# Kernel optimization log

Measured on AMD Instinct MI355X. Metric: run time of the kernel, lower is better.

## Reference

```python
import jax, jax.numpy as jnp
import numpy as np

V = 6          # num_variables
K = 6          # codebook_size
D = 32         # embedding_dim
C = 3          # channels
B = 64         # batch
N = K ** V     # 46656 codebook combinations
EPS = 1e-5     # torch BatchNorm eps
ENTROPY_SCALE = 0.1


def setup_inputs() -> dict:
    key = jax.random.key(0)
    ks = jax.random.split(key, 40)
    i = iter(range(40))
    def rn(shape, s):
        return jax.random.normal(ks[next(i)], shape, dtype=jnp.float32) * s
    def rv(shape):
        return 0.5 + 0.5 * jax.random.uniform(ks[next(i)], shape, dtype=jnp.float32)
    inp = {
        'x': jax.random.normal(ks[next(i)], (B, C, 7, 7), dtype=jnp.float32),
        # encoder
        'conv_w': rn((256, C, 7, 7), 0.08), 'conv_b': rn((256,), 0.01),
        'ebn2_g': 1.0 + rn((256,), 0.1), 'ebn2_b': rn((256,), 0.1),
        'fc1_w': rn((1024, 256), 0.06), 'fc1_b': rn((1024,), 0.01),
        'ebn1_g': 1.0 + rn((1024,), 0.1), 'ebn1_b': rn((1024,), 0.1),
        'fc2_w': rn((V * K, 1024), 0.03), 'fc2_b': rn((V * K,), 0.01),
        # quantizer embeddings (V separate codebooks)
        'embeds': jax.random.normal(ks[next(i)], (V, K, D), dtype=jnp.float32),
        # decoder
        'dfc1_w': rn((1024, V * D), 0.07), 'dfc1_b': rn((1024,), 0.01),
        'dbn1_g': 1.0 + rn((1024,), 0.1), 'dbn1_b': rn((1024,), 0.1),
        'dbn1_rm': rn((1024,), 0.1), 'dbn1_rv': rv((1024,)),
        'dfc2_w': rn((256, 1024), 0.03), 'dfc2_b': rn((256,), 0.01),
        'dbn2_g': 1.0 + rn((256,), 0.1), 'dbn2_b': rn((256,), 0.1),
        'dbn2_rm': rn((256,), 0.1), 'dbn2_rv': rv((256,)),
        'dct1_w': rn((256, 16, 7, 7), 0.05), 'dct1_b': rn((16,), 0.01),
        'dbn3_g': 1.0 + rn((16,), 0.1), 'dbn3_b': rn((16,), 0.1),
        'dbn3_rm': rn((16,), 0.1), 'dbn3_rv': rv((16,)),
        'dct2_w': rn((16, C), 0.2), 'dct2_b': rn((C,), 0.01),
    }
    return inp


def _bn_eval(t, g, b, rm, rvar):
    # eval-mode BatchNorm (running stats); params broadcast over leading dims
    return g * (t - rm) * jax.lax.rsqrt(rvar + EPS) + b


def _bn_train(t, g, b):
    # train-mode BatchNorm1d on (B, F): biased batch statistics over dim 0
    m = t.mean(0)
    v = ((t - m) ** 2).mean(0)
    return g * (t - m) * jax.lax.rsqrt(v + EPS) + b


def _decode_all(embeds, dfc1_w, dfc1_b, dbn1_g, dbn1_b, dbn1_rm, dbn1_rv,
                dfc2_w, dfc2_b, dbn2_g, dbn2_b, dbn2_rm, dbn2_rv,
                dct1_w, dct1_b, dbn3_g, dbn3_b, dbn3_rm, dbn3_rv,
                dct2_w, dct2_b):
    # enumerate all K^V index tuples in itertools.product order (first var slowest)
    idx = jnp.arange(N)
    powers = K ** (V - 1 - jnp.arange(V))
    combos = (idx[:, None] // powers[None, :]) % K          # (N, V)
    z = embeds[jnp.arange(V)[None, :], combos]              # (N, V, D) gather
    h = z.reshape(N, V * D) @ dfc1_w.T + dfc1_b             # (N, 1024)
    h = jax.nn.relu(_bn_eval(h, dbn1_g, dbn1_b, dbn1_rm, dbn1_rv))
    h = h @ dfc2_w.T + dfc2_b                               # (N, 256)
    h = jax.nn.relu(_bn_eval(h, dbn2_g, dbn2_b, dbn2_rm, dbn2_rv))
    # ConvTranspose2d(256,16,7,stride=2) on 1x1 input == einsum with full kernel
    h = jnp.einsum('ni,iohw->nohw', h, dct1_w) + dct1_b[:, None, None]  # (N,16,7,7)
    h = jax.nn.relu(_bn_eval(h, dbn3_g[:, None, None], dbn3_b[:, None, None],
                             dbn3_rm[:, None, None], dbn3_rv[:, None, None]))
    # ConvTranspose2d(16,C,1,1) == pointwise channel mix
    em = jnp.einsum('nihw,io->nohw', h, dct2_w) + dct2_b[:, None, None]  # (N,C,7,7)
    return em


def reference(x, conv_w, conv_b, ebn2_g, ebn2_b, fc1_w, fc1_b, ebn1_g, ebn1_b,
              fc2_w, fc2_b, embeds, dfc1_w, dfc1_b, dbn1_g, dbn1_b, dbn1_rm,
              dbn1_rv, dfc2_w, dfc2_b, dbn2_g, dbn2_b, dbn2_rm, dbn2_rv,
              dct1_w, dct1_b, dbn3_g, dbn3_b, dbn3_rm, dbn3_rv, dct2_w, dct2_b):
    # emission means for every codebook combination (batched decode, BN eval)
    em = _decode_all(embeds, dfc1_w, dfc1_b, dbn1_g, dbn1_b, dbn1_rm, dbn1_rv,
                     dfc2_w, dfc2_b, dbn2_g, dbn2_b, dbn2_rm, dbn2_rv,
                     dct1_w, dct1_b, dbn3_g, dbn3_b, dbn3_rm, dbn3_rv,
                     dct2_w, dct2_b)                         # (N, C, 7, 7)
    # encoder: Conv2d(C,256,7) on 7x7 input collapses to a single GEMM
    e = jnp.einsum('bchw,ochw->bo', x, conv_w) + conv_b      # (B, 256)
    e = jax.nn.relu(_bn_train(e, ebn2_g, ebn2_b))
    e = e @ fc1_w.T + fc1_b                                  # (B, 1024)
    e = jax.nn.relu(_bn_train(e, ebn1_g, ebn1_b))
    logits = e @ fc2_w.T + fc2_b                             # (B, V*K)
    # quantizer
    latent_dist = jax.nn.softmax(logits.reshape(B, V, K), axis=-1)
    latent_loss = ENTROPY_SCALE * jnp.sum(
        latent_dist * jnp.log(latent_dist + 1e-10), axis=(1, 2))
    # obs logits: -0.5 * ||em - x||^2 summed over (C,H,W), via expanded form
    E = em.reshape(N, -1)                                    # (N, 147)
    X = x.reshape(B, -1)                                     # (B, 147)
    obs = -0.5 * (jnp.sum(E * E, -1)[None, :]
                  - 2.0 * (X @ E.T)
                  + jnp.sum(X * X, -1)[:, None])             # (B, N)
    obs_logits = obs.reshape((B,) + (K,) * V)
    return obs_logits, latent_dist, latent_loss
```

## Files before the change

### kernel.cpp

```cpp
#include <hip/hip_runtime.h>
#include <math.h>

#define EPSF 1e-5f
#define NNC 46656

typedef __attribute__((ext_vector_type(4))) float  f32x4;
typedef __attribute__((ext_vector_type(8))) short  short8;
typedef __attribute__((ext_vector_type(8))) unsigned short ushort8;
typedef __attribute__((ext_vector_type(4))) unsigned int uint4v;

__device__ __forceinline__ float bf2f(unsigned short u) {
    unsigned int x = ((unsigned int)u) << 16;
    return __builtin_bit_cast(float, x);
}
__device__ __forceinline__ unsigned short f2bf(float f) {
    unsigned int x = __builtin_bit_cast(unsigned int, f);
    unsigned int r = (x + 0x7fffu + ((x >> 16) & 1u)) >> 16;
    return (unsigned short)r;
}

__device__ __forceinline__ short8 packrelu8(ushort8 H8, ushort8 S8) {
    uint4v H = __builtin_bit_cast(uint4v, H8);
    uint4v S = __builtin_bit_cast(uint4v, S8);
    uint4v O;
#pragma unroll
    for (int d = 0; d < 4; ++d) {
        float hlo = __builtin_bit_cast(float, H[d] << 16);
        float hhi = __builtin_bit_cast(float, H[d] & 0xffff0000u);
        float slo = __builtin_bit_cast(float, S[d] << 16);
        float shi = __builtin_bit_cast(float, S[d] & 0xffff0000u);
        unsigned int rlo = __builtin_bit_cast(unsigned int, fmaxf(hlo + slo, 0.f));
        unsigned int rhi = __builtin_bit_cast(unsigned int, fmaxf(hhi + shi, 0.f));
        O[d] = __builtin_amdgcn_perm(rhi, rlo, 0x07060302u);
    }
    return __builtin_bit_cast(short8, O);
}

#define WS_SH    37888u
#define WS_S3    148480u
#define WS_W2BF  259072u
#define WS_C2    390144u
#define WS_W3BF  390400u
#define WS_C3    490752u
#define WS_XBF   490768u
#define WS_SX2   495888u
#define WS_E1T   495952u
#define WS_E2T   512336u
#define WS_FLAG  577872u

#define OBS_SIZE (64*NNC)
#define DIST_OFF OBS_SIZE
#define LOSS_OFF (OBS_SIZE + 64*36)

#define LDS_BYTES 75008


__global__ void dvae_k1(const float* __restrict__ x,
                        const float* __restrict__ conv_w, const float* __restrict__ conv_b,
                        const float* __restrict__ ebn2_g, const float* __restrict__ ebn2_b,
                        const float* __restrict__ embeds, const float* __restrict__ dfc1_w,
                        const float* __restrict__ dfc1_b,
                        const float* __restrict__ dbn1_g, const float* __restrict__ dbn1_b,
                        const float* __restrict__ dbn1_rm, const float* __restrict__ dbn1_rv,
                        const float* __restrict__ dfc2_w, const float* __restrict__ dfc2_b,
                        const float* __restrict__ dbn2_g, const float* __restrict__ dbn2_b,
                        const float* __restrict__ dbn2_rm, const float* __restrict__ dbn2_rv,
                        const float* __restrict__ dct1_w, const float* __restrict__ dct1_b,
                        const float* __restrict__ dbn3_g, const float* __restrict__ dbn3_b,
                        const float* __restrict__ dbn3_rm, const float* __restrict__ dbn3_rv,
                        float* __restrict__ ws) {
    __shared__ float sbuf[12544];
    int bx = blockIdx.x, tid = threadIdx.x;
    if (bx < 64) {
        float* wtile = sbuf;
        float* semb  = sbuf + 3088;
        float* Pt    = sbuf + 4240;
        float* c1s   = sbuf + 4960;
        int j0 = bx * 16;
        for (int e = tid; e < 16 * 192; e += 256)
            wtile[(e / 192) * 193 + (e % 192)] = dfc1_w[j0 * 192 + e];
        for (int e = tid; e < 1152; e += 256) semb[e] = embeds[e];
        __syncthreads();
        for (int e = tid; e < 576; e += 256) {
            int vk = e >> 4, jL = e & 15;
            int v = vk / 6;
            int j = j0 + jL;
            const float* wrow = &wtile[jL * 193 + v * 32];
            const float* ep = &semb[vk * 32];
            float dot = 0.f;
#pragma unroll
            for (int d = 0; d < 32; ++d) dot += wrow[d] * ep[d];
            float s1 = dbn1_g[j] * rsqrtf(dbn1_rv[j] + EPSF);
            Pt[vk * 20 + jL] = s1 * dot;
        }
        if (tid < 16) {
            int j = j0 + tid;
            float s = dbn1_g[j] * rsqrtf(dbn1_rv[j] + EPSF);
            c1s[tid] = s * dfc1_b[j] + dbn1_b[j] - dbn1_rm[j] * s;
        }
        __syncthreads();
        unsigned short* Sh = (unsigned short*)(ws + WS_SH);
        unsigned short* S3 = (unsigned short*)(ws + WS_S3);
        for (int e = tid; e < 216 * 16; e += 256) {
            int gh = e >> 4, jL = e & 15;
            int d0 = gh / 36, d1 = (gh / 6) % 6, d2 = gh % 6;
            float vh = c1s[jL] + Pt[d0 * 20 + jL] + Pt[(6 + d1) * 20 + jL] + Pt[(12 + d2) * 20 + jL];
            float vs = Pt[(18 + d0) * 20 + jL] + Pt[(24 + d1) * 20 + jL] + Pt[(30 + d2) * 20 + jL];
            Sh[gh * 1024 + j0 + jL] = f2bf(vh);
            S3[gh * 1024 + j0 + jL] = f2bf(vs);
        }
    } else if (bx < 320) {
        int t = (bx - 64) * 256 + tid;
        int i = t >> 8, kq = (t & 255) * 4;
        float s2 = dbn2_g[i] * rsqrtf(dbn2_rv[i] + EPSF);
        float4 w = *(const float4*)(dfc2_w + i * 1024 + kq);
        unsigned short* dst = (unsigned short*)(ws + WS_W2BF) + i * 1024 + kq;
        dst[0] = f2bf(s2 * w.x); dst[1] = f2bf(s2 * w.y);
        dst[2] = f2bf(s2 * w.z); dst[3] = f2bf(s2 * w.w);
        if (kq == 0) ws[WS_C2 + i] = s2 * dfc2_b[i] + dbn2_b[i] - dbn2_rm[i] * s2;
    } else if (bx < 336) {
        int blk = bx - 320;
        for (int e = tid; e < 12544; e += 256) sbuf[e] = dct1_w[blk * 12544 + e];
        __syncthreads();
        unsigned short* W3 = (unsigned short*)(ws + WS_W3BF);
        for (int e = tid; e < 1568; e += 256) {
            int up = e >> 1, k8 = (e & 1) * 8;
            int o = up & 15, hw = up >> 4;
            float s3 = dbn3_g[o] * rsqrtf(dbn3_rv[o] + EPSF);
            ushort8 ov;
#pragma unroll
            for (int t2 = 0; t2 < 8; ++t2)
                ov[t2] = f2bf(s3 * sbuf[(k8 + t2) * 784 + o * 49 + hw]);
            *(ushort8*)(W3 + up * 256 + blk * 16 + k8) = ov;
        }
        if (blk == 0 && tid < 16) {
            float s = dbn3_g[tid] * rsqrtf(dbn3_rv[tid] + EPSF);
            ws[WS_C3 + tid] = s * dct1_b[tid] + dbn3_b[tid] - dbn3_rm[tid] * s;
        }
    } else if (bx == 336) {
        unsigned short* Xb = (unsigned short*)(ws + WS_XBF);
        if (tid == 0) *(int*)(ws + WS_FLAG) = 0;
        if (tid < 64) {
            const float* xp = x + tid * 147;
            float s = 0.f;
            for (int qq = 0; qq < 147; ++qq) { float v = xp[qq]; s += v * v; }
            ws[WS_SX2 + tid] = s;
        }
        for (int e = tid; e < 64 * 160; e += 256) {
            int b = e / 160, col = e % 160;
            float v = 0.f;
            if (col < 147) { int hw = col / 3, c = col % 3; v = x[b * 147 + c * 49 + hw]; }
            Xb[e] = f2bf(v);
        }
    } else {
        int blk = bx - 337;
        for (int e = tid; e < 9408; e += 256) sbuf[e] = x[e];
        __syncthreads();
        int b = tid & 63;
        int oL = __builtin_amdgcn_readfirstlane(tid >> 6);
        int o = blk * 4 + oL;
        const float* wp = conv_w + o * 147;
        float acc = conv_b[o];
#pragma unroll 7
        for (int qq = 0; qq < 147; ++qq) acc += sbuf[b * 147 + qq] * wp[qq];
        float m = acc;
#pragma unroll
        for (int s = 1; s < 64; s <<= 1) m += __shfl_xor(m, s);
        m *= (1.f / 64.f);
        float d = acc - m;
        float var = d * d;
#pragma unroll
        for (int s = 1; s < 64; s <<= 1) var += __shfl_xor(var, s);
        var *= (1.f / 64.f);
        float y = ebn2_g[o] * d * rsqrtf(var + EPSF) + ebn2_b[o];
        ws[WS_E1T + o * 64 + b] = fmaxf(y, 0.f);
    }
}


__launch_bounds__(256, 2)
__global__ void dvae_k3(const unsigned short* __restrict__ Sh,
                        const unsigned short* __restrict__ S3g,
                        const unsigned short* __restrict__ W2,
                        const float* __restrict__ c2g,
                        const unsigned short* __restrict__ W3,
                        const float* __restrict__ c3g,
                        const float* __restrict__ d2wg,
                        const float* __restrict__ d2bg,
                        const unsigned short* __restrict__ Xg,
                        const float* __restrict__ sx2g,
                        const float* __restrict__ fc1_w, const float* __restrict__ fc1_b,
                        const float* __restrict__ ebn1_g, const float* __restrict__ ebn1_b,
                        const float* __restrict__ e1T,
                        float* __restrict__ e2T,
                        int* __restrict__ flag,
                        const float* __restrict__ fc2_w,
                        const float* __restrict__ fc2_b,
                        float* __restrict__ out) {
    extern __shared__ char sm[];
    int tid = threadIdx.x;

    if (blockIdx.x < 256) {
        int blk = blockIdx.x;
        int b = tid & 63;
        int jL = __builtin_amdgcn_readfirstlane(tid >> 6);
        int j = blk * 4 + jL;
        const float* wp = fc1_w + j * 256;
        float acc = fc1_b[j];
#pragma unroll 8
        for (int o = 0; o < 256; ++o) acc += e1T[o * 64 + b] * wp[o];
        float m = acc;
#pragma unroll
        for (int s = 1; s < 64; s <<= 1) m += __shfl_xor(m, s);
        m *= (1.f / 64.f);
        float d = acc - m;
        float var = d * d;
#pragma unroll
        for (int s = 1; s < 64; s <<= 1) var += __shfl_xor(var, s);
        var *= (1.f / 64.f);
        float y = ebn1_g[j] * d * rsqrtf(var + EPSF) + ebn1_b[j];
        e2T[j * 64 + b] = fmaxf(y, 0.f);
        __syncthreads();
        if (tid == 0) { __threadfence(); atomicAdd(flag, 1); }
        return;
    }

    if (blockIdx.x == 256) {
        if (tid == 0) {
            while (atomicAdd(flag, 0) < 256) __builtin_amdgcn_s_sleep(8);
        }
        __syncthreads();
        float* wch = (float*)sm;
        float* ech = (float*)(sm + 18432);
        float* LG  = (float*)(sm + 51200);
        int b = tid & 63;
        int wvU = __builtin_amdgcn_readfirstlane(tid >> 6);
        float accv[9];
#pragma unroll
        for (int it = 0; it < 9; ++it) accv[it] = 0.f;
        for (int ch = 0; ch < 8; ++ch) {
            __syncthreads();
            for (int e = tid; e < 36 * 128; e += 256)
                wch[e] = fc2_w[(e >> 7) * 1024 + ch * 128 + (e & 127)];
            for (int e = tid; e < 128 * 64; e += 256)
                ech[e] = e2T[(ch * 128 + (e >> 6)) * 64 + (e & 63)];
            __syncthreads();
            for (int jl = 0; jl < 128; ++jl) {
                float ev = ech[jl * 64 + b];
#pragma unroll
                for (int it = 0; it < 9; ++it)
                    accv[it] += ev * wch[(wvU + it * 4) * 128 + jl];
            }
        }
#pragma unroll
        for (int it = 0; it < 9; ++it) {
            int o = wvU + it * 4;
            LG[b * 36 + o] = accv[it] + fc2_b[o];
        }
        __syncthreads();
        if (tid < 64) {
            float loss = 0.f;
#pragma unroll
            for (int v = 0; v < 6; ++v) {
                float mx = -1e30f;
#pragma unroll
                for (int k = 0; k < 6; ++k) mx = fmaxf(mx, LG[tid * 36 + v * 6 + k]);
                float s = 0.f, ex[6];
#pragma unroll
                for (int k = 0; k < 6; ++k) { ex[k] = expf(LG[tid * 36 + v * 6 + k] - mx); s += ex[k]; }
                float inv = 1.f / s;
#pragma unroll
                for (int k = 0; k < 6; ++k) {
                    float dd = ex[k] * inv;
                    out[DIST_OFF + tid * 36 + v * 6 + k] = dd;
                    loss += dd * logf(dd + 1e-10f);
                }
            }
            out[LOSS_OFF + tid] = 0.1f * loss;
        }
        return;
    }

    int wv = tid >> 6, lane = tid & 63, l15 = lane & 15, q = lane >> 4;
    int db = blockIdx.x - 257;
    int g0 = (db / 27) * 8, r0 = (db % 27) * 8;
    float* sE2p = (float*)(sm + 0);
    float* sE2f = (float*)(sm + 1024);
    unsigned short* emL = (unsigned short*)(sm + 1280);
    float* h3w = (float*)(sm + 21760 + wv * 5120);
    unsigned short* h2L = (unsigned short*)(sm + 42240);
    char* Ast = sm + 1280;

    f32x4 acc[4][4];
#pragma unroll
    for (int a = 0; a < 4; ++a)
#pragma unroll
        for (int b = 0; b < 4; ++b) acc[a][b] = (f32x4){0.f, 0.f, 0.f, 0.f};

    int gh_t = g0 + (lane >> 3);
    int r_t  = r0 + (lane & 7);
    const unsigned short* shp = Sh  + gh_t * 1024 + wv * 32;
    const unsigned short* s3p = S3g + r_t  * 1024 + wv * 32;
    const unsigned short* bbase = W2 + (wv * 64 + l15) * 1024 + q * 8;
    int Xw = (lane & 7) << 4;
    int Xr = (l15 & 7) << 4;

    ushort8 rsh[4], rs3[4];
#pragma unroll
    for (int i = 0; i < 4; ++i) {
        rsh[i] = *(const ushort8*)(shp + i * 8);
        rs3[i] = *(const ushort8*)(s3p + i * 8);
    }
    short8 bpre[4];
#pragma unroll
    for (int j = 0; j < 4; ++j) bpre[j] = *(const short8*)(bbase + j * 16384);
#pragma unroll
    for (int i = 0; i < 4; ++i)
        *(short8*)(Ast + lane * 256 + ((wv * 64 + i * 16) ^ Xw)) = packrelu8(rsh[i], rs3[i]);
    __syncthreads();

    for (int c = 0; c < 8; ++c) {
        int cb = (c & 1) << 14;
        if (c < 7) {
            const unsigned short* p1 = shp + (c + 1) * 128;
            const unsigned short* p3 = s3p + (c + 1) * 128;
#pragma unroll
            for (int i = 0; i < 4; ++i) {
                rsh[i] = *(const ushort8*)(p1 + i * 8);
                rs3[i] = *(const ushort8*)(p3 + i * 8);
            }
        }
#pragma unroll
        for (int ss = 0; ss < 4; ++ss) {
            int s = c * 4 + ss;
            short8 af[4];
#pragma unroll
            for (int mt = 0; mt < 4; ++mt)
                af[mt] = *(const short8*)(Ast + cb + (mt * 16 + l15) * 256 + ((ss * 64 + q * 16) ^ Xr));
            short8 bcur[4];
#pragma unroll
            for (int j = 0; j < 4; ++j) bcur[j] = bpre[j];
            if (s < 31) {
#pragma unroll
                for (int j = 0; j < 4; ++j) bpre[j] = *(const short8*)(bbase + j * 16384 + (s + 1) * 32);
            }
#pragma unroll
            for (int mt = 0; mt < 4; ++mt)
#pragma unroll
                for (int j = 0; j < 4; ++j)
                    acc[mt][j] = __builtin_amdgcn_mfma_f32_16x16x32_bf16(af[mt], bcur[j], acc[mt][j], 0, 0, 0);
        }
        if (c < 7) {
            int nb = ((c + 1) & 1) << 14;
#pragma unroll
            for (int i = 0; i < 4; ++i)
                *(short8*)(Ast + nb + lane * 256 + ((wv * 64 + i * 16) ^ Xw)) = packrelu8(rsh[i], rs3[i]);
        }
        __syncthreads();
    }

#pragma unroll
    for (int j = 0; j < 4; ++j) {
        int i = wv * 64 + j * 16 + l15;
        float cc = c2g[i];
#pragma unroll
        for (int mt = 0; mt < 4; ++mt)
#pragma unroll
            for (int r = 0; r < 4; ++r) {
                int m = mt * 16 + q * 4 + r;
                h2L[((i >> 3) * 64 + m) * 8 + (i & 7)] = f2bf(fmaxf(acc[mt][j][r] + cc, 0.f));
            }
    }
    __syncthreads();

    float c3v = c3g[l15];
    float db0 = d2bg[0], db1 = d2bg[1], db2 = d2bg[2];
    float dw0[16], dw1[16], dw2[16];
#pragma unroll
    for (int o = 0; o < 16; ++o) {
        dw0[o] = d2wg[o * 3 + 0]; dw1[o] = d2wg[o * 3 + 1]; dw2[o] = d2wg[o * 3 + 2];
    }
    float sE2a = 0.f;
    for (int c = wv; c < 13; c += 4) {
        int hw0 = c * 4;
        f32x4 a2[4][4];
#pragma unroll
        for (int a = 0; a < 4; ++a)
#pragma unroll
            for (int b = 0; b < 4; ++b) a2[a][b] = (f32x4){0.f, 0.f, 0.f, 0.f};
        const unsigned short* b3[4];
#pragma unroll
        for (int j = 0; j < 4; ++j) {
            int hw = hw0 + j; if (hw > 48) hw = 48;
            b3[j] = W3 + (hw * 16 + l15) * 256 + q * 8;
        }
        short8 bpre2[4];
#pragma unroll
        for (int j = 0; j < 4; ++j) bpre2[j] = *(const short8*)(b3[j]);
#pragma unroll
        for (int s = 0; s < 8; ++s) {
            short8 bcur[4];
#pragma unroll
            for (int j = 0; j < 4; ++j) bcur[j] = bpre2[j];
            if (s < 7) {
#pragma unroll
                for (int j = 0; j < 4; ++j) bpre2[j] = *(const short8*)(b3[j] + (s + 1) * 32);
            }
            short8 af[4];
#pragma unroll
            for (int mt = 0; mt < 4; ++mt)
                af[mt] = *(const short8*)(h2L + ((s * 4 + q) * 64 + mt * 16 + l15) * 8);
#pragma unroll
            for (int mt = 0; mt < 4; ++mt)
#pragma unroll
                for (int j = 0; j < 4; ++j)
                    a2[mt][j] = __builtin_amdgcn_mfma_f32_16x16x32_bf16(af[mt], bcur[j], a2[mt][j], 0, 0, 0);
        }
#pragma unroll
        for (int j = 0; j < 4; ++j) {
            int hw = hw0 + j;
            if (hw <= 48) {
#pragma unroll
                for (int mt = 0; mt < 4; ++mt)
#pragma unroll
                    for (int r = 0; r < 4; ++r)
                        h3w[(mt * 16 + q * 4 + r) * 20 + l15] = fmaxf(a2[mt][j][r] + c3v, 0.f);
                float hvv[16];
#pragma unroll
                for (int g = 0; g < 4; ++g) {
                    f32x4 tv = *(const f32x4*)(h3w + lane * 20 + g * 4);
                    hvv[g * 4 + 0] = tv[0]; hvv[g * 4 + 1] = tv[1];
                    hvv[g * 4 + 2] = tv[2]; hvv[g * 4 + 3] = tv[3];
                }
                float e0 = db0, e1 = db1, e2 = db2;
#pragma unroll
                for (int o = 0; o < 16; ++o) {
                    e0 += hvv[o] * dw0[o]; e1 += hvv[o] * dw1[o]; e2 += hvv[o] * dw2[o];
                }
                unsigned short u0 = f2bf(e0), u1 = f2bf(e1), u2 = f2bf(e2);
                float f0 = bf2f(u0), f1 = bf2f(u1), f2v = bf2f(u2);
                sE2a += f0 * f0 + f1 * f1 + f2v * f2v;
                emL[lane * 160 + hw * 3 + 0] = u0;
                emL[lane * 160 + hw * 3 + 1] = u1;
                emL[lane * 160 + hw * 3 + 2] = u2;
            }
        }
    }
    sE2p[wv * 64 + lane] = sE2a;
    for (int e = tid; e < 64 * 13; e += 256) emL[(e / 13) * 160 + 147 + (e % 13)] = 0;
    __syncthreads();
    if (tid < 64) sE2f[tid] = sE2p[tid] + sE2p[64 + tid] + sE2p[128 + tid] + sE2p[192 + tid];
    __syncthreads();

    f32x4 aO[4];
#pragma unroll
    for (int j = 0; j < 4; ++j) aO[j] = (f32x4){0.f, 0.f, 0.f, 0.f};
    const unsigned short* xrow = Xg + (wv * 16 + l15) * 160 + q * 8;
#pragma unroll
    for (int s = 0; s < 5; ++s) {
        short8 af = *(const short8*)(xrow + s * 32);
#pragma unroll
        for (int j = 0; j < 4; ++j) {
            short8 bfv = *(const short8*)(emL + (j * 16 + l15) * 160 + s * 32 + q * 8);
            aO[j] = __builtin_amdgcn_mfma_f32_16x16x32_bf16(af, bfv, aO[j], 0, 0, 0);
        }
    }
    int b0 = wv * 16 + q * 4;
    float sxv[4];
#pragma unroll
    for (int r = 0; r < 4; ++r) sxv[r] = sx2g[b0 + r];
#pragma unroll
    for (int j = 0; j < 4; ++j) {
        int rloc = j * 16 + l15;
        int n = (g0 + (rloc >> 3)) * 216 + r0 + (rloc & 7);
        float he = 0.5f * sE2f[rloc];
#pragma unroll
        for (int r = 0; r < 4; ++r)
            out[(size_t)(b0 + r) * NNC + n] = aO[j][r] - he - 0.5f * sxv[r];
    }
}


extern "C" void kernel_launch(void* const* d_in, const int* in_sizes, int n_in,
                              void* d_out, int out_size, void* d_ws, size_t ws_size,
                              hipStream_t stream) {
    const float* x       = (const float*)d_in[0];
    const float* conv_w  = (const float*)d_in[1];
    const float* conv_b  = (const float*)d_in[2];
    const float* ebn2_g  = (const float*)d_in[3];
    const float* ebn2_b  = (const float*)d_in[4];
    const float* fc1_w   = (const float*)d_in[5];
    const float* fc1_b   = (const float*)d_in[6];
    const float* ebn1_g  = (const float*)d_in[7];
    const float* ebn1_b  = (const float*)d_in[8];
    const float* fc2_w   = (const float*)d_in[9];
    const float* fc2_b   = (const float*)d_in[10];
    const float* embeds  = (const float*)d_in[11];
    const float* dfc1_w  = (const float*)d_in[12];
    const float* dfc1_b  = (const float*)d_in[13];
    const float* dbn1_g  = (const float*)d_in[14];
    const float* dbn1_b  = (const float*)d_in[15];
    const float* dbn1_rm = (const float*)d_in[16];
    const float* dbn1_rv = (const float*)d_in[17];
    const float* dfc2_w  = (const float*)d_in[18];
    const float* dfc2_b  = (const float*)d_in[19];
    const float* dbn2_g  = (const float*)d_in[20];
    const float* dbn2_b  = (const float*)d_in[21];
    const float* dbn2_rm = (const float*)d_in[22];
    const float* dbn2_rv = (const float*)d_in[23];
    const float* dct1_w  = (const float*)d_in[24];
    const float* dct1_b  = (const float*)d_in[25];
    const float* dbn3_g  = (const float*)d_in[26];
    const float* dbn3_b  = (const float*)d_in[27];
    const float* dbn3_rm = (const float*)d_in[28];
    const float* dbn3_rv = (const float*)d_in[29];
    const float* dct2_w  = (const float*)d_in[30];
    const float* dct2_b  = (const float*)d_in[31];

    float* ws  = (float*)d_ws;
    float* out = (float*)d_out;

    dvae_k1<<<401, 256, 0, stream>>>(x, conv_w, conv_b, ebn2_g, ebn2_b,
                                     embeds, dfc1_w, dfc1_b, dbn1_g, dbn1_b, dbn1_rm, dbn1_rv,
                                     dfc2_w, dfc2_b, dbn2_g, dbn2_b, dbn2_rm, dbn2_rv,
                                     dct1_w, dct1_b, dbn3_g, dbn3_b, dbn3_rm, dbn3_rv, ws);

    hipFuncSetAttribute(reinterpret_cast<const void*>(dvae_k3),
                        hipFuncAttributeMaxDynamicSharedMemorySize, LDS_BYTES);
    dvae_k3<<<986, 256, LDS_BYTES, stream>>>(
        (const unsigned short*)(ws + WS_SH), (const unsigned short*)(ws + WS_S3),
        (const unsigned short*)(ws + WS_W2BF), ws + WS_C2,
        (const unsigned short*)(ws + WS_W3BF), ws + WS_C3,
        dct2_w, dct2_b,
        (const unsigned short*)(ws + WS_XBF), ws + WS_SX2,
        fc1_w, fc1_b, ebn1_g, ebn1_b,
        ws + WS_E1T, ws + WS_E2T, (int*)(ws + WS_FLAG),
        fc2_w, fc2_b, out);
}
```

Before: 260.6 us.

## Fuse final 16-to-3 projection into MFMA registers and shrink LDS for occupancy

The A/B operands of the third decoder MFMA are swapped, so each lane holds four output channels for one codebook row. The final 16-to-3 transposed-conv projection is then done in registers with cross-quarter shuffles, which removes the per-wave h3w LDS staging buffer. LDS regions are re-aliased (emL at offset 0, sE2p over h2L, LG over wch), the LDS footprint drops, and launch bounds rise to three blocks per CU. The aliasing requires extra barriers and leaves only a quarter of lanes active for the bf16 stores, and the higher occupancy target may force register spilling.

```diff
diff --git a/kernel.cpp b/kernel.cpp
--- a/kernel.cpp
+++ b/kernel.cpp
@@ -52,7 +52,7 @@
 #define DIST_OFF OBS_SIZE
 #define LOSS_OFF (OBS_SIZE + 64*36)
 
-#define LDS_BYTES 75008
+#define LDS_BYTES 53248
 
 
 __global__ void dvae_k1(const float* __restrict__ x,
@@ -178,7 +178,7 @@
 }
 
 
-__launch_bounds__(256, 2)
+__launch_bounds__(256, 3)
 __global__ void dvae_k3(const unsigned short* __restrict__ Sh,
                         const unsigned short* __restrict__ S3g,
                         const unsigned short* __restrict__ W2,
@@ -232,7 +232,7 @@
         __syncthreads();
         float* wch = (float*)sm;
         float* ech = (float*)(sm + 18432);
-        float* LG  = (float*)(sm + 51200);
+        float* LG  = (float*)sm;
         int b = tid & 63;
         int wvU = __builtin_amdgcn_readfirstlane(tid >> 6);
         float accv[9];
@@ -252,6 +252,7 @@
                     accv[it] += ev * wch[(wvU + it * 4) * 128 + jl];
             }
         }
+        __syncthreads();
 #pragma unroll
         for (int it = 0; it < 9; ++it) {
             int o = wvU + it * 4;
@@ -284,12 +285,11 @@
     int wv = tid >> 6, lane = tid & 63, l15 = lane & 15, q = lane >> 4;
     int db = blockIdx.x - 257;
     int g0 = (db / 27) * 8, r0 = (db % 27) * 8;
-    float* sE2p = (float*)(sm + 0);
-    float* sE2f = (float*)(sm + 1024);
-    unsigned short* emL = (unsigned short*)(sm + 1280);
-    float* h3w = (float*)(sm + 21760 + wv * 5120);
-    unsigned short* h2L = (unsigned short*)(sm + 42240);
-    char* Ast = sm + 1280;
+    unsigned short* emL = (unsigned short*)sm;
+    unsigned short* h2L = (unsigned short*)(sm + 20480);
+    float* sE2p = (float*)(sm + 20480);
+    float* sE2f = (float*)(sm + 21504);
+    char* Ast = sm;
 
     f32x4 acc[4][4];
 #pragma unroll
@@ -373,14 +373,18 @@
     }
     __syncthreads();
 
-    float c3v = c3g[l15];
+    float c3q[4], dwq0[4], dwq1[4], dwq2[4];
+#pragma unroll
+    for (int r = 0; r < 4; ++r) {
+        int o = q * 4 + r;
+        c3q[r]  = c3g[o];
+        dwq0[r] = d2wg[o * 3 + 0];
+        dwq1[r] = d2wg[o * 3 + 1];
+        dwq2[r] = d2wg[o * 3 + 2];
+    }
     float db0 = d2bg[0], db1 = d2bg[1], db2 = d2bg[2];
-    float dw0[16], dw1[16], dw2[16];
-#pragma unroll
-    for (int o = 0; o < 16; ++o) {
-        dw0[o] = d2wg[o * 3 + 0]; dw1[o] = d2wg[o * 3 + 1]; dw2[o] = d2wg[o * 3 + 2];
-    }
-    float sE2a = 0.f;
+    float sE2acc[4] = {0.f, 0.f, 0.f, 0.f};
+
     for (int c = wv; c < 13; c += 4) {
         int hw0 = c * 4;
         f32x4 a2[4][4];
@@ -414,39 +418,39 @@
             for (int mt = 0; mt < 4; ++mt)
 #pragma unroll
                 for (int j = 0; j < 4; ++j)
-                    a2[mt][j] = __builtin_amdgcn_mfma_f32_16x16x32_bf16(af[mt], bcur[j], a2[mt][j], 0, 0, 0);
+                    a2[mt][j] = __builtin_amdgcn_mfma_f32_16x16x32_bf16(bcur[j], af[mt], a2[mt][j], 0, 0, 0);
         }
 #pragma unroll
         for (int j = 0; j < 4; ++j) {
             int hw = hw0 + j;
             if (hw <= 48) {
 #pragma unroll
-                for (int mt = 0; mt < 4; ++mt)
-#pragma unroll
-                    for (int r = 0; r < 4; ++r)
-                        h3w[(mt * 16 + q * 4 + r) * 20 + l15] = fmaxf(a2[mt][j][r] + c3v, 0.f);
-                float hvv[16];
-#pragma unroll
-                for (int g = 0; g < 4; ++g) {
-                    f32x4 tv = *(const f32x4*)(h3w + lane * 20 + g * 4);
-                    hvv[g * 4 + 0] = tv[0]; hvv[g * 4 + 1] = tv[1];
-                    hvv[g * 4 + 2] = tv[2]; hvv[g * 4 + 3] = tv[3];
+                for (int mt = 0; mt < 4; ++mt) {
+                    float p0 = 0.f, p1 = 0.f, p2 = 0.f;
+#pragma unroll
+                    for (int r = 0; r < 4; ++r) {
+                        float h = fmaxf(a2[mt][j][r] + c3q[r], 0.f);
+                        p0 += h * dwq0[r]; p1 += h * dwq1[r]; p2 += h * dwq2[r];
+                    }
+                    p0 += __shfl_xor(p0, 16); p0 += __shfl_xor(p0, 32);
+                    p1 += __shfl_xor(p1, 16); p1 += __shfl_xor(p1, 32);
+                    p2 += __shfl_xor(p2, 16); p2 += __shfl_xor(p2, 32);
+                    unsigned short u0 = f2bf(p0 + db0), u1 = f2bf(p1 + db1), u2 = f2bf(p2 + db2);
+                    float f0 = bf2f(u0), f1 = bf2f(u1), f2v = bf2f(u2);
+                    if (q == 0) {
+                        sE2acc[mt] += f0 * f0 + f1 * f1 + f2v * f2v;
+                        unsigned short* er = emL + (mt * 16 + l15) * 160 + hw * 3;
+                        er[0] = u0; er[1] = u1; er[2] = u2;
+                    }
                 }
-                float e0 = db0, e1 = db1, e2 = db2;
-#pragma unroll
-                for (int o = 0; o < 16; ++o) {
-                    e0 += hvv[o] * dw0[o]; e1 += hvv[o] * dw1[o]; e2 += hvv[o] * dw2[o];
-                }
-                unsigned short u0 = f2bf(e0), u1 = f2bf(e1), u2 = f2bf(e2);
-                float f0 = bf2f(u0), f1 = bf2f(u1), f2v = bf2f(u2);
-                sE2a += f0 * f0 + f1 * f1 + f2v * f2v;
-                emL[lane * 160 + hw * 3 + 0] = u0;
-                emL[lane * 160 + hw * 3 + 1] = u1;
-                emL[lane * 160 + hw * 3 + 2] = u2;
-            }
-        }
-    }
-    sE2p[wv * 64 + lane] = sE2a;
+            }
+        }
+    }
+    __syncthreads();
+    if (q == 0) {
+#pragma unroll
+        for (int mt = 0; mt < 4; ++mt) sE2p[wv * 64 + mt * 16 + l15] = sE2acc[mt];
+    }
     for (int e = tid; e < 64 * 13; e += 256) emL[(e / 13) * 160 + 147 + (e % 13)] = 0;
     __syncthreads();
     if (tid < 64) sE2f[tid] = sE2p[tid] + sE2p[64 + tid] + sE2p[128 + tid] + sE2p[192 + tid];
```

Result: no change. 259.1 us (-0.6%).
